# Kernel optimization log

Hardware: AMD Instinct MI355X
Metric: run time of the kernel (lower is better)

Reference implementation:

```python
import jax, jax.numpy as jnp
import numpy as np

B, T, D, H, C = 128, 256, 256, 1024, 10


def setup_inputs() -> dict:
    key = jax.random.key(0)
    ks = jax.random.split(key, 11)
    std = 1.0 / T  # matches nn.init.normal_(std=1/seq_length)
    inp = {
        'x':   jax.random.normal(ks[0], (B, T, D), dtype=jnp.float32),
        'Wfx': jax.random.normal(ks[1], (D, H), dtype=jnp.float32) * std,
        'Wix': jax.random.normal(ks[2], (D, H), dtype=jnp.float32) * std,
        'Wgx': jax.random.normal(ks[3], (D, H), dtype=jnp.float32) * std,
        'Wox': jax.random.normal(ks[4], (D, H), dtype=jnp.float32) * std,
        'Wfh': jax.random.normal(ks[5], (H, H), dtype=jnp.float32) * std,
        'Wih': jax.random.normal(ks[6], (H, H), dtype=jnp.float32) * std,
        'Wgh': jax.random.normal(ks[7], (H, H), dtype=jnp.float32) * std,
        'Woh': jax.random.normal(ks[8], (H, H), dtype=jnp.float32) * std,
        'bf':  jnp.zeros((H,), jnp.float32),
        'bi':  jnp.zeros((H,), jnp.float32),
        'bg':  jnp.zeros((H,), jnp.float32),
        'bo':  jnp.zeros((H,), jnp.float32),
        'Wph': jax.random.normal(ks[9], (H, C), dtype=jnp.float32) * std,
        'bp':  jnp.zeros((C,), jnp.float32),
    }
    return inp


def reference(x, Wfx, Wix, Wgx, Wox, Wfh, Wih, Wgh, Woh, bf, bi, bg, bo, Wph, bp):
    b, t, d = x.shape
    h = Wfh.shape[0]
    # Fuse the 4 input-side and 4 hidden-side matmuls into two big GEMMs per step
    Wx = jnp.concatenate([Wfx, Wix, Wgx, Wox], axis=1)  # [D, 4H]
    Wh = jnp.concatenate([Wfh, Wih, Wgh, Woh], axis=1)  # [H, 4H]
    bb = jnp.concatenate([bf, bi, bg, bo])              # [4H]

    # Precompute all input projections in one batched GEMM: [T, B, 4H]
    xg = jnp.einsum('btd,dk->tbk', x, Wx) + bb

    def step(carry, xgt):
        hs, cs = carry
        gates = xgt + hs @ Wh  # [B, 4H]
        f = jax.nn.sigmoid(gates[:, 0 * h:1 * h])
        i = jax.nn.sigmoid(gates[:, 1 * h:2 * h])
        g = jnp.tanh(gates[:, 2 * h:3 * h])
        o = jax.nn.sigmoid(gates[:, 3 * h:4 * h])
        cs = g * i + cs * f
        hs = jnp.tanh(cs) * o
        return (hs, cs), None

    h0 = jnp.zeros((b, h), x.dtype)
    c0 = jnp.zeros((b, h), x.dtype)
    (hT, _), _ = jax.lax.scan(step, (h0, c0), xg)
    return hT @ Wph + bp
```

## Files before the change

### kernel.cpp

```cpp
#include <hip/hip_runtime.h>
#include <math.h>


#define BB 128
#define TT 256
#define DD 256
#define HH 1024
#define NKT 40
#define KHT 20
#define PF 4

typedef __bf16 bf16x8 __attribute__((ext_vector_type(8)));
typedef float  f32x4  __attribute__((ext_vector_type(4)));
typedef unsigned short u16;
typedef u16 u16x8 __attribute__((ext_vector_type(8)));

__device__ __forceinline__ u16 f2bf(float f){
  unsigned u = __builtin_bit_cast(unsigned, f);
  u += 0x7fffu + ((u >> 16) & 1u);
  return (u16)(u >> 16);
}
__device__ __forceinline__ float bf2f(u16 b){
  unsigned u = ((unsigned)b) << 16;
  return __builtin_bit_cast(float, u);
}

__global__ void prep_wpack(const float* __restrict__ Wfx, const float* __restrict__ Wix,
                           const float* __restrict__ Wgx, const float* __restrict__ Wox,
                           const float* __restrict__ Wfh, const float* __restrict__ Wih,
                           const float* __restrict__ Wgh, const float* __restrict__ Woh,
                           u16* __restrict__ Wpack){
  int id = blockIdx.x * 256 + threadIdx.x;
  int lane = id & 63;
  int kt = (id >> 6) % NKT;
  int ct = id / (64 * NKT);
  int col = ct * 16 + (lane & 15);
  int g = col >> 10, n = col & 1023;
  int kbase = kt * 32 + (lane >> 4) * 8;
  const float* Wx = (g==0) ? Wfx : (g==1) ? Wix : (g==2) ? Wgx : Wox;
  const float* Wh = (g==0) ? Wfh : (g==1) ? Wih : (g==2) ? Wgh : Woh;
  u16x8 v;
  #pragma unroll
  for (int j = 0; j < 8; ++j){
    int k = kbase + j;
    float f = (k < DD) ? Wx[k * HH + n] : Wh[(k - DD) * HH + n];
    v[j] = f2bf(f);
  }
  *(u16x8*)(Wpack + (size_t)id * 8) = v;
}

__global__ void prep_xT(const float* __restrict__ x, u16* __restrict__ xT){
  int id = blockIdx.x * 256 + threadIdx.x;
  int t = id >> 12;
  int b = (id >> 5) & 127;
  int d0 = (id & 31) * 8;
  const float* src = x + ((size_t)b * TT + t) * DD + d0;
  u16x8 v;
  #pragma unroll
  for (int j = 0; j < 8; ++j) v[j] = f2bf(src[j]);
  *(u16x8*)(xT + (size_t)id * 8) = v;
}

__global__ __launch_bounds__(512) void lstm_step(
    const u16* __restrict__ xTt,
    const u16* __restrict__ Wpack,
    const u16* __restrict__ hin,
    u16* __restrict__ hout,
    float* __restrict__ cbuf,
    const float* __restrict__ bfv, const float* __restrict__ biv,
    const float* __restrict__ bgv, const float* __restrict__ bov){
  __shared__ u16x8 As4[NKT * 64];
  __shared__ float gLds[16][132];
  __shared__ float pLds[16][132];
  const int tid = threadIdx.x;
  const int n0 = blockIdx.x * 32;
  const int m0 = blockIdx.y * 16;

  const int w = tid >> 6, lane = tid & 63, cr = lane & 15, q4 = lane >> 4;
  const int g  = w & 3;
  const int kh = w >> 2;
  const int ktBeg = kh * KHT;

  const size_t ct0 = (size_t)(g * 64 + blockIdx.x * 2);
  const u16x8* Wp = (const u16x8*)Wpack;
  const u16x8* wq0 = Wp + ct0 * NKT * 64 + lane;
  const u16x8* wq1 = wq0 + NKT * 64;

  u16x8 aP[PF], b0P[PF], b1P[PF];
  #pragma unroll
  for (int i = 0; i < PF; ++i){
    b0P[i] = wq0[(size_t)(ktBeg + i) * 64];
    b1P[i] = wq1[(size_t)(ktBeg + i) * 64];
  }

  #pragma unroll
  for (int it = 0; it < 5; ++it){
    int ch = tid + it * 512;
    int m = ch / 160;
    int k0 = (ch - m * 160) * 8;
    const u16* src = (k0 < DD) ? (xTt + (m0 + m) * DD + k0)
                               : (hin + (m0 + m) * HH + (k0 - DD));
    u16x8 val = *(const u16x8*)src;
    int kt = k0 >> 5, q = (k0 >> 3) & 3;
    As4[kt * 64 + 16 * q + m] = val;
  }
  __syncthreads();

  #pragma unroll
  for (int i = 0; i < PF; ++i) aP[i] = As4[(ktBeg + i) * 64 + lane];

  f32x4 acc0 = {0.f, 0.f, 0.f, 0.f}, acc1 = {0.f, 0.f, 0.f, 0.f};
  #pragma unroll
  for (int kt = 0; kt < KHT; ++kt){
    const int slot = kt & (PF - 1);
    u16x8 ac = aP[slot], b0 = b0P[slot], b1 = b1P[slot];
    if (kt + PF < KHT){
      aP[slot]  = As4[(ktBeg + kt + PF) * 64 + lane];
      b0P[slot] = wq0[(size_t)(ktBeg + kt + PF) * 64];
      b1P[slot] = wq1[(size_t)(ktBeg + kt + PF) * 64];
    }
    acc0 = __builtin_amdgcn_mfma_f32_16x16x32_bf16(__builtin_bit_cast(bf16x8, ac),
             __builtin_bit_cast(bf16x8, b0), acc0, 0, 0, 0);
    acc1 = __builtin_amdgcn_mfma_f32_16x16x32_bf16(__builtin_bit_cast(bf16x8, ac),
             __builtin_bit_cast(bf16x8, b1), acc1, 0, 0, 0);
  }

  if (kh){
    #pragma unroll
    for (int r = 0; r < 4; ++r){
      pLds[q4 * 4 + r][g * 32 + cr]      = acc0[r];
      pLds[q4 * 4 + r][g * 32 + 16 + cr] = acc1[r];
    }
  }
  __syncthreads();
  if (!kh){
    const float* bptr = (g==0) ? bfv : (g==1) ? biv : (g==2) ? bgv : bov;
    float bias0 = bptr[n0 + cr], bias1 = bptr[n0 + 16 + cr];
    #pragma unroll
    for (int r = 0; r < 4; ++r){
      gLds[q4 * 4 + r][g * 32 + cr] =
          acc0[r] + pLds[q4 * 4 + r][g * 32 + cr] + bias0;
      gLds[q4 * 4 + r][g * 32 + 16 + cr] =
          acc1[r] + pLds[q4 * 4 + r][g * 32 + 16 + cr] + bias1;
    }
  }
  __syncthreads();

  {
    int row = tid >> 5, nn = tid & 31;
    float fp = gLds[row][nn],      ip = gLds[row][32 + nn];
    float gp = gLds[row][64 + nn], op = gLds[row][96 + nn];
    float fs = 1.f / (1.f + expf(-fp));
    float is = 1.f / (1.f + expf(-ip));
    float gs = tanhf(gp);
    float os = 1.f / (1.f + expf(-op));
    int gi = (m0 + row) * HH + n0 + nn;
    float cn = gs * is + cbuf[gi] * fs;
    cbuf[gi] = cn;
    hout[gi] = f2bf(tanhf(cn) * os);
  }
}

__global__ void final_proj(const u16* __restrict__ h, const float* __restrict__ Wph,
                           const float* __restrict__ bp, float* __restrict__ out){
  __shared__ float red[10][256];
  int b = blockIdx.x, tid = threadIdx.x;
  float p[10];
  #pragma unroll
  for (int c = 0; c < 10; ++c) p[c] = 0.f;
  for (int k = tid; k < HH; k += 256){
    float hv = bf2f(h[b * HH + k]);
    const float* wr = Wph + (size_t)k * 10;
    #pragma unroll
    for (int c = 0; c < 10; ++c) p[c] += hv * wr[c];
  }
  #pragma unroll
  for (int c = 0; c < 10; ++c) red[c][tid] = p[c];
  __syncthreads();
  for (int s = 128; s > 0; s >>= 1){
    if (tid < s){
      #pragma unroll
      for (int c = 0; c < 10; ++c) red[c][tid] += red[c][tid + s];
    }
    __syncthreads();
  }
  if (tid < 10) out[b * 10 + tid] = red[tid][0] + bp[tid];
}

extern "C" void kernel_launch(void* const* d_in, const int* in_sizes, int n_in,
                              void* d_out, int out_size, void* d_ws, size_t ws_size,
                              hipStream_t stream){
  (void)in_sizes; (void)n_in; (void)out_size; (void)ws_size;
  const float* x   = (const float*)d_in[0];
  const float* Wfx = (const float*)d_in[1];
  const float* Wix = (const float*)d_in[2];
  const float* Wgx = (const float*)d_in[3];
  const float* Wox = (const float*)d_in[4];
  const float* Wfh = (const float*)d_in[5];
  const float* Wih = (const float*)d_in[6];
  const float* Wgh = (const float*)d_in[7];
  const float* Woh = (const float*)d_in[8];
  const float* bfv = (const float*)d_in[9];
  const float* biv = (const float*)d_in[10];
  const float* bgv = (const float*)d_in[11];
  const float* bov = (const float*)d_in[12];
  const float* Wph = (const float*)d_in[13];
  const float* bp  = (const float*)d_in[14];

  char* ws = (char*)d_ws;
  u16*  Wpack = (u16*)ws;
  u16*  xT    = (u16*)(ws + 10485760);
  u16*  h0    = (u16*)(ws + 27262976);
  u16*  h1    = (u16*)(ws + 27525120);
  float* cb   = (float*)(ws + 27787264);

  prep_wpack<<<2560, 256, 0, stream>>>(Wfx, Wix, Wgx, Wox, Wfh, Wih, Wgh, Woh, Wpack);
  prep_xT<<<4096, 256, 0, stream>>>(x, xT);
  hipMemsetAsync(h0, 0, 262144, stream);
  hipMemsetAsync(cb, 0, 524288, stream);

  for (int t = 0; t < TT; ++t){
    const u16* hin = (t & 1) ? h1 : h0;
    u16*       hout = (t & 1) ? h0 : h1;
    lstm_step<<<dim3(32, 8), 512, 0, stream>>>(xT + (size_t)t * BB * DD, Wpack,
                                               hin, hout, cb, bfv, biv, bgv, bov);
  }
  final_proj<<<128, 256, 0, stream>>>(h0, Wph, bp, (float*)d_out);
}
```

Before: 1.984 ms.

## Replace per-step launches with persistent cooperative LSTM kernel and row-group barriers

Runs the whole 256-step recurrence in one cooperative kernel of 512 blocks. Each block keeps its 40 bf16 weight fragments in registers and its cell state in a register. Blocks sync per step through atomic counters scoped to each batch-row group, which removes 256 kernel launches and repeated weight reloads. It also adds a swizzled LDS layout, fast exp-based sigmoid/tanh and x-prefetch overlap. The costs are heavy register pressure, spin-wait barrier latency, and a dependence on co-residency (there is a fallback to the old path).

```diff
diff --git a/kernel.cpp b/kernel.cpp
--- a/kernel.cpp
+++ b/kernel.cpp
@@ -24,6 +24,21 @@
   unsigned u = ((unsigned)b) << 16;
   return __builtin_bit_cast(float, u);
 }
+__device__ __forceinline__ float sigm(float x){
+  return 1.f / (1.f + __expf(-x));
+}
+__device__ __forceinline__ float tanh_fast(float x){
+  return 2.f / (1.f + __expf(-2.f * x)) - 1.f;
+}
+__device__ __forceinline__ int swz(int slot){
+  return slot ^ ((slot >> 6) & 7) ^ (((slot >> 4) & 1) << 2);
+}
+
+#define KLIST40(F) F(0) F(1) F(2) F(3) F(4) F(5) F(6) F(7) F(8) F(9) \
+  F(10) F(11) F(12) F(13) F(14) F(15) F(16) F(17) F(18) F(19) \
+  F(20) F(21) F(22) F(23) F(24) F(25) F(26) F(27) F(28) F(29) \
+  F(30) F(31) F(32) F(33) F(34) F(35) F(36) F(37) F(38) F(39)
+#define SLIST10(F) F(0) F(1) F(2) F(3) F(4) F(5) F(6) F(7) F(8) F(9)
 
 __global__ void prep_wpack(const float* __restrict__ Wfx, const float* __restrict__ Wix,
                            const float* __restrict__ Wgx, const float* __restrict__ Wox,
@@ -61,11 +76,116 @@
   *(u16x8*)(xT + (size_t)id * 8) = v;
 }
 
+__global__ __launch_bounds__(256, 2) void lstm_persist(
+    const u16* __restrict__ xT, const u16* __restrict__ Wpack,
+    u16* __restrict__ h0, u16* __restrict__ h1,
+    const float* __restrict__ bfv, const float* __restrict__ biv,
+    const float* __restrict__ bgv, const float* __restrict__ bov,
+    unsigned* __restrict__ barCnt){
+  __shared__ u16x8 As4[NKT * 64];
+  __shared__ float gLds[16][68];
+  const int tid = threadIdx.x;
+  const int bx = blockIdx.x >> 3;
+  const int by = blockIdx.x & 7;
+  const int n0 = bx * 16;
+  const int m0 = by * 16;
+  unsigned* const myCnt = barCnt + by * 32;
+
+  const int g = tid >> 6;
+  const int lane = tid & 63, cr = lane & 15, q4 = lane >> 4;
+
+  const u16x8* wq = (const u16x8*)Wpack + (size_t)(g * 64 + bx) * NKT * 64 + lane;
+#define DECLW(i) u16x8 w_##i;
+  KLIST40(DECLW)
+#define LOADW(i) w_##i = wq[(size_t)(i) * 64];
+  KLIST40(LOADW)
+#define PINW(i) asm("" : "+v"(w_##i));
+  KLIST40(PINW)
+
+  const float* bptr = (g==0) ? bfv : (g==1) ? biv : (g==2) ? bgv : bov;
+  const float bias = bptr[n0 + cr];
+
+  unsigned isx = 0;
+#define SGEOM(i) int so##i, sd##i; { int ch = tid + (i) * 256; \
+    int m = ch / 160; int k0 = (ch - m * 160) * 8; \
+    if (k0 < DD){ so##i = (m0 + m) * DD + k0; isx |= (1u << (i)); } \
+    else        { so##i = (m0 + m) * HH + (k0 - DD); } \
+    sd##i = swz((k0 >> 5) * 64 + 16 * ((k0 >> 3) & 3) + m); }
+  SLIST10(SGEOM)
+#define STX(i) if ((isx >> (i)) & 1)   As4[sd##i] = *(const u16x8*)(xnext + so##i);
+#define STH(i) if (!((isx >> (i)) & 1)) As4[sd##i] = *(const u16x8*)(hnext + so##i);
+
+  const int crow = tid >> 4, cnn = tid & 15;
+  const int gi = (m0 + crow) * HH + n0 + cnn;
+  float cstate = 0.f;
+
+  {
+    const u16* xnext = xT;
+    const u16* hnext = h0;
+    SLIST10(STX)
+    SLIST10(STH)
+  }
+
+  #pragma unroll 1
+  for (int t = 0; t < TT; ++t){
+    u16* hout = (t & 1) ? h0 : h1;
+    __syncthreads();
+
+    f32x4 accA = {0.f, 0.f, 0.f, 0.f}, accB = {0.f, 0.f, 0.f, 0.f};
+    u16x8 a0 = As4[swz(0 * 64 + lane)];
+    u16x8 a1 = As4[swz(1 * 64 + lane)];
+    u16x8 a2 = As4[swz(2 * 64 + lane)];
+    u16x8 a3 = As4[swz(3 * 64 + lane)];
+#define AS(i) (((i)&3)==0 ? a0 : ((i)&3)==1 ? a1 : ((i)&3)==2 ? a2 : a3)
+#define STEPK(i) { u16x8 ac = AS(i); \
+    if ((i) + 4 < NKT){ int ld = swz(((i) + 4) * 64 + lane); \
+      if (((i)&3)==0) a0 = As4[ld]; else if (((i)&3)==1) a1 = As4[ld]; \
+      else if (((i)&3)==2) a2 = As4[ld]; else a3 = As4[ld]; } \
+    if ((i) & 1) accB = __builtin_amdgcn_mfma_f32_16x16x32_bf16( \
+        __builtin_bit_cast(bf16x8, ac), __builtin_bit_cast(bf16x8, w_##i), accB, 0, 0, 0); \
+    else accA = __builtin_amdgcn_mfma_f32_16x16x32_bf16( \
+        __builtin_bit_cast(bf16x8, ac), __builtin_bit_cast(bf16x8, w_##i), accA, 0, 0, 0); }
+    KLIST40(STEPK)
+
+    #pragma unroll
+    for (int r = 0; r < 4; ++r)
+      gLds[q4 * 4 + r][g * 16 + cr] = accA[r] + accB[r] + bias;
+    __syncthreads();
+
+    if (t + 1 < TT){
+      const u16* xnext = xT + (size_t)(t + 1) * BB * DD;
+      SLIST10(STX)
+    }
+
+    {
+      float fp = gLds[crow][cnn],      ip = gLds[crow][16 + cnn];
+      float gp = gLds[crow][32 + cnn], op = gLds[crow][48 + cnn];
+      cstate = tanh_fast(gp) * sigm(ip) + cstate * sigm(fp);
+      hout[gi] = f2bf(tanh_fast(cstate) * sigm(op));
+    }
+
+    if (t != TT - 1){
+      __syncthreads();
+      if (tid == 0){
+        __threadfence();
+        __hip_atomic_fetch_add(myCnt, 1u, __ATOMIC_RELAXED,
+                               __HIP_MEMORY_SCOPE_AGENT);
+        const unsigned tgt = (unsigned)(t + 1) * 64u;
+        while (__hip_atomic_load(myCnt, __ATOMIC_RELAXED,
+                                 __HIP_MEMORY_SCOPE_AGENT) < tgt)
+          __builtin_amdgcn_s_sleep(2);
+        __threadfence();
+      }
+      __syncthreads();
+      const u16* hnext = hout;
+      SLIST10(STH)
+    }
+  }
+}
+
 __global__ __launch_bounds__(512) void lstm_step(
-    const u16* __restrict__ xTt,
-    const u16* __restrict__ Wpack,
-    const u16* __restrict__ hin,
-    u16* __restrict__ hout,
+    const u16* __restrict__ xTt, const u16* __restrict__ Wpack,
+    const u16* __restrict__ hin, u16* __restrict__ hout,
     float* __restrict__ cbuf,
     const float* __restrict__ bfv, const float* __restrict__ biv,
     const float* __restrict__ bgv, const float* __restrict__ bov){
@@ -213,17 +333,33 @@
   u16*  h0    = (u16*)(ws + 27262976);
   u16*  h1    = (u16*)(ws + 27525120);
   float* cb   = (float*)(ws + 27787264);
+  unsigned* barCnt = (unsigned*)(ws + 27787264);
 
   prep_wpack<<<2560, 256, 0, stream>>>(Wfx, Wix, Wgx, Wox, Wfh, Wih, Wgh, Woh, Wpack);
   prep_xT<<<4096, 256, 0, stream>>>(x, xT);
   hipMemsetAsync(h0, 0, 262144, stream);
-  hipMemsetAsync(cb, 0, 524288, stream);
-
-  for (int t = 0; t < TT; ++t){
-    const u16* hin = (t & 1) ? h1 : h0;
-    u16*       hout = (t & 1) ? h0 : h1;
-    lstm_step<<<dim3(32, 8), 512, 0, stream>>>(xT + (size_t)t * BB * DD, Wpack,
-                                               hin, hout, cb, bfv, biv, bgv, bov);
-  }
+
+  int nb = 0;
+  hipError_t qe = hipOccupancyMaxActiveBlocksPerMultiprocessor(
+      &nb, (const void*)lstm_persist, 256, 0);
+  hipError_t ce = hipErrorUnknown;
+  if (qe == hipSuccess && nb >= 2){
+    hipMemsetAsync(barCnt, 0, 1024, stream);
+    void* args[] = {(void*)&xT, (void*)&Wpack, (void*)&h0, (void*)&h1,
+                    (void*)&bfv, (void*)&biv, (void*)&bgv, (void*)&bov,
+                    (void*)&barCnt};
+    ce = hipLaunchCooperativeKernel((const void*)lstm_persist, dim3(512),
+                                    dim3(256), args, 0, stream);
+  }
+  if (ce != hipSuccess){
+    hipMemsetAsync(cb, 0, 524288, stream);
+    for (int t = 0; t < TT; ++t){
+      const u16* hin  = (t & 1) ? h1 : h0;
+      u16*       hout = (t & 1) ? h0 : h1;
+      lstm_step<<<dim3(32, 8), 512, 0, stream>>>(xT + (size_t)t * BB * DD, Wpack,
+                                                 hin, hout, cb, bfv, biv, bgv, bov);
+    }
+  }
+
   final_proj<<<128, 256, 0, stream>>>(h0, Wph, bp, (float*)d_out);
 }
```

Measured after the change: 1.981 ms. No clear change (-0.1%).

## Retile LSTM step to 32x16 blocks sharing weight fragments across two row tiles

Applied to the files above, without the earlier changes.

Each block of the per-step LSTM kernel now covers 32 batch rows by 16 hidden units per gate instead of 16 by 32, and the grid changes from 32x8 to 64x4. Each weight fragment loaded from global memory now feeds two MFMAs over two 16-row A tiles, so weight traffic per step is halved. The A operand moves to a swizzled shared-memory layout, and weight prefetch depth goes up to 8. The cost is twice the activation staging per block, and the wider gather of h and x per block may add latency.

```diff
diff --git a/kernel.cpp b/kernel.cpp
--- a/kernel.cpp
+++ b/kernel.cpp
@@ -8,7 +8,8 @@
 #define HH 1024
 #define NKT 40
 #define KHT 20
-#define PF 4
+#define PFB 8
+#define PFA 4
 
 typedef __bf16 bf16x8 __attribute__((ext_vector_type(8)));
 typedef float  f32x4  __attribute__((ext_vector_type(4)));
@@ -23,6 +24,9 @@
 __device__ __forceinline__ float bf2f(u16 b){
   unsigned u = ((unsigned)b) << 16;
   return __builtin_bit_cast(float, u);
+}
+__device__ __forceinline__ int swz2(int slot){
+  return slot ^ ((slot >> 7) & 7);
 }
 
 __global__ void prep_wpack(const float* __restrict__ Wfx, const float* __restrict__ Wix,
@@ -61,7 +65,7 @@
   *(u16x8*)(xT + (size_t)id * 8) = v;
 }
 
-__global__ __launch_bounds__(512) void lstm_step(
+__global__ __launch_bounds__(512) void lstm_step2(
     const u16* __restrict__ xTt,
     const u16* __restrict__ Wpack,
     const u16* __restrict__ hin,
@@ -69,92 +73,92 @@
     float* __restrict__ cbuf,
     const float* __restrict__ bfv, const float* __restrict__ biv,
     const float* __restrict__ bgv, const float* __restrict__ bov){
-  __shared__ u16x8 As4[NKT * 64];
-  __shared__ float gLds[16][132];
-  __shared__ float pLds[16][132];
+  __shared__ u16x8 As4[NKT * 128];
+  __shared__ float pLds[32][68];
+  __shared__ float gLds[32][68];
   const int tid = threadIdx.x;
-  const int n0 = blockIdx.x * 32;
-  const int m0 = blockIdx.y * 16;
+  const int bx = blockIdx.x;
+  const int n0 = bx * 16;
+  const int m0 = blockIdx.y * 32;
 
   const int w = tid >> 6, lane = tid & 63, cr = lane & 15, q4 = lane >> 4;
   const int g  = w & 3;
   const int kh = w >> 2;
   const int ktBeg = kh * KHT;
 
-  const size_t ct0 = (size_t)(g * 64 + blockIdx.x * 2);
-  const u16x8* Wp = (const u16x8*)Wpack;
-  const u16x8* wq0 = Wp + ct0 * NKT * 64 + lane;
-  const u16x8* wq1 = wq0 + NKT * 64;
-
-  u16x8 aP[PF], b0P[PF], b1P[PF];
-  #pragma unroll
-  for (int i = 0; i < PF; ++i){
-    b0P[i] = wq0[(size_t)(ktBeg + i) * 64];
-    b1P[i] = wq1[(size_t)(ktBeg + i) * 64];
-  }
-
-  #pragma unroll
-  for (int it = 0; it < 5; ++it){
+  const u16x8* wq = (const u16x8*)Wpack + (size_t)(g * 64 + bx) * NKT * 64 + lane;
+  u16x8 bP[PFB];
+  #pragma unroll
+  for (int i = 0; i < PFB; ++i) bP[i] = wq[(size_t)(ktBeg + i) * 64];
+
+  #pragma unroll
+  for (int it = 0; it < 10; ++it){
     int ch = tid + it * 512;
-    int m = ch / 160;
-    int k0 = (ch - m * 160) * 8;
-    const u16* src = (k0 < DD) ? (xTt + (m0 + m) * DD + k0)
-                               : (hin + (m0 + m) * HH + (k0 - DD));
+    int mr = ch / 160;
+    int k0 = (ch - mr * 160) * 8;
+    const u16* src = (k0 < DD) ? (xTt + (m0 + mr) * DD + k0)
+                               : (hin + (m0 + mr) * HH + (k0 - DD));
     u16x8 val = *(const u16x8*)src;
-    int kt = k0 >> 5, q = (k0 >> 3) & 3;
-    As4[kt * 64 + 16 * q + m] = val;
-  }
-  __syncthreads();
-
-  #pragma unroll
-  for (int i = 0; i < PF; ++i) aP[i] = As4[(ktBeg + i) * 64 + lane];
-
-  f32x4 acc0 = {0.f, 0.f, 0.f, 0.f}, acc1 = {0.f, 0.f, 0.f, 0.f};
-  #pragma unroll
-  for (int kt = 0; kt < KHT; ++kt){
-    const int slot = kt & (PF - 1);
-    u16x8 ac = aP[slot], b0 = b0P[slot], b1 = b1P[slot];
-    if (kt + PF < KHT){
-      aP[slot]  = As4[(ktBeg + kt + PF) * 64 + lane];
-      b0P[slot] = wq0[(size_t)(ktBeg + kt + PF) * 64];
-      b1P[slot] = wq1[(size_t)(ktBeg + kt + PF) * 64];
-    }
-    acc0 = __builtin_amdgcn_mfma_f32_16x16x32_bf16(__builtin_bit_cast(bf16x8, ac),
-             __builtin_bit_cast(bf16x8, b0), acc0, 0, 0, 0);
-    acc1 = __builtin_amdgcn_mfma_f32_16x16x32_bf16(__builtin_bit_cast(bf16x8, ac),
-             __builtin_bit_cast(bf16x8, b1), acc1, 0, 0, 0);
+    int slot = (k0 >> 5) * 128 + (mr >> 4) * 64 + ((k0 >> 3) & 3) * 16 + (mr & 15);
+    As4[swz2(slot)] = val;
+  }
+  __syncthreads();
+
+  u16x8 aA[PFA], aB[PFA];
+  #pragma unroll
+  for (int i = 0; i < PFA; ++i){
+    aA[i] = As4[swz2((ktBeg + i) * 128 + lane)];
+    aB[i] = As4[swz2((ktBeg + i) * 128 + 64 + lane)];
+  }
+
+  f32x4 accA = {0.f, 0.f, 0.f, 0.f}, accB = {0.f, 0.f, 0.f, 0.f};
+  #pragma unroll
+  for (int i = 0; i < KHT; ++i){
+    u16x8 b  = bP[i & (PFB - 1)];
+    u16x8 a0 = aA[i & (PFA - 1)];
+    u16x8 a1 = aB[i & (PFA - 1)];
+    if (i + PFB < KHT)
+      bP[i & (PFB - 1)] = wq[(size_t)(ktBeg + i + PFB) * 64];
+    if (i + PFA < KHT){
+      aA[i & (PFA - 1)] = As4[swz2((ktBeg + i + PFA) * 128 + lane)];
+      aB[i & (PFA - 1)] = As4[swz2((ktBeg + i + PFA) * 128 + 64 + lane)];
+    }
+    accA = __builtin_amdgcn_mfma_f32_16x16x32_bf16(__builtin_bit_cast(bf16x8, a0),
+             __builtin_bit_cast(bf16x8, b), accA, 0, 0, 0);
+    accB = __builtin_amdgcn_mfma_f32_16x16x32_bf16(__builtin_bit_cast(bf16x8, a1),
+             __builtin_bit_cast(bf16x8, b), accB, 0, 0, 0);
   }
 
   if (kh){
     #pragma unroll
     for (int r = 0; r < 4; ++r){
-      pLds[q4 * 4 + r][g * 32 + cr]      = acc0[r];
-      pLds[q4 * 4 + r][g * 32 + 16 + cr] = acc1[r];
+      pLds[q4 * 4 + r][g * 16 + cr]      = accA[r];
+      pLds[16 + q4 * 4 + r][g * 16 + cr] = accB[r];
     }
   }
   __syncthreads();
   if (!kh){
     const float* bptr = (g==0) ? bfv : (g==1) ? biv : (g==2) ? bgv : bov;
-    float bias0 = bptr[n0 + cr], bias1 = bptr[n0 + 16 + cr];
+    const float bias = bptr[n0 + cr];
     #pragma unroll
     for (int r = 0; r < 4; ++r){
-      gLds[q4 * 4 + r][g * 32 + cr] =
-          acc0[r] + pLds[q4 * 4 + r][g * 32 + cr] + bias0;
-      gLds[q4 * 4 + r][g * 32 + 16 + cr] =
-          acc1[r] + pLds[q4 * 4 + r][g * 32 + 16 + cr] + bias1;
+      gLds[q4 * 4 + r][g * 16 + cr] =
+          accA[r] + pLds[q4 * 4 + r][g * 16 + cr] + bias;
+      gLds[16 + q4 * 4 + r][g * 16 + cr] =
+          accB[r] + pLds[16 + q4 * 4 + r][g * 16 + cr] + bias;
     }
   }
   __syncthreads();
 
   {
-    int row = tid >> 5, nn = tid & 31;
-    float fp = gLds[row][nn],      ip = gLds[row][32 + nn];
-    float gp = gLds[row][64 + nn], op = gLds[row][96 + nn];
+    int crow = tid >> 4, cnn = tid & 15;
+    float fp = gLds[crow][cnn],      ip = gLds[crow][16 + cnn];
+    float gp = gLds[crow][32 + cnn], op = gLds[crow][48 + cnn];
     float fs = 1.f / (1.f + expf(-fp));
     float is = 1.f / (1.f + expf(-ip));
     float gs = tanhf(gp);
     float os = 1.f / (1.f + expf(-op));
-    int gi = (m0 + row) * HH + n0 + nn;
+    int gi = (m0 + crow) * HH + n0 + cnn;
     float cn = gs * is + cbuf[gi] * fs;
     cbuf[gi] = cn;
     hout[gi] = f2bf(tanhf(cn) * os);
@@ -220,10 +224,10 @@
   hipMemsetAsync(cb, 0, 524288, stream);
 
   for (int t = 0; t < TT; ++t){
-    const u16* hin = (t & 1) ? h1 : h0;
+    const u16* hin  = (t & 1) ? h1 : h0;
     u16*       hout = (t & 1) ? h0 : h1;
-    lstm_step<<<dim3(32, 8), 512, 0, stream>>>(xT + (size_t)t * BB * DD, Wpack,
-                                               hin, hout, cb, bfv, biv, bgv, bov);
+    lstm_step2<<<dim3(64, 4), 512, 0, stream>>>(xT + (size_t)t * BB * DD, Wpack,
+                                                hin, hout, cb, bfv, biv, bgv, bov);
   }
   final_proj<<<128, 256, 0, stream>>>(h0, Wph, bp, (float*)d_out);
 }
```

New measurement: 2.150 ms. +8.4%, slower.
